# Optimization experiments

Measured on AMD Instinct MI355X. Metric: run time of the kernel, lower is better.

Reference implementation:

```python
import jax, jax.numpy as jnp
import numpy as np

B, IN_DIM, CTRL, N_LOC, LOC_SZ, OUT = 2048, 512, 512, 65536, 64, 1
EPS = 1e-8


def setup_inputs() -> dict:
    key = jax.random.key(0)
    ks = jax.random.split(key, 11)
    s = 0.02
    return {
        "x": jax.random.normal(ks[0], (B, IN_DIM), dtype=jnp.float32),
        # Controller: h = tanh(x W_h + b_h), gate = x W_g + b_g
        "W_h": jax.random.normal(ks[1], (IN_DIM, CTRL), dtype=jnp.float32) * s,
        "b_h": jnp.zeros((CTRL,), dtype=jnp.float32),
        "W_g": jax.random.normal(ks[2], (IN_DIM, 1), dtype=jnp.float32) * s,
        "b_g": jnp.zeros((1,), dtype=jnp.float32),
        # Head read-key net: key = tanh(h W_k + b_k)
        "W_k": jax.random.normal(ks[3], (CTRL, LOC_SZ), dtype=jnp.float32) * s,
        "b_k": jnp.zeros((LOC_SZ,), dtype=jnp.float32),
        # Memory matrix [locations, location_size]
        "M": jax.random.normal(ks[4], (N_LOC, LOC_SZ), dtype=jnp.float32),
        # Output linear: (ctrl_dim + location_size) -> output_dim
        "W_out": jax.random.normal(ks[5], (CTRL + LOC_SZ, OUT), dtype=jnp.float32) * s,
        "b_out": jnp.zeros((OUT,), dtype=jnp.float32),
    }


def reference(x, W_h, b_h, W_g, b_g, W_k, b_k, M, W_out, b_out):
    # Vectorized version of the original per-sample Python loop.
    h = jnp.tanh(x @ W_h + b_h)                # [B, ctrl_dim]
    gate = x @ W_g + b_g                       # [B, 1]
    read_key = jnp.tanh(h @ W_k + b_k)         # [B, loc_sz]
    # Cosine-similarity content addressing over memory rows.
    kn = read_key / (jnp.linalg.norm(read_key, axis=-1, keepdims=True) + EPS)
    Mn = M / (jnp.linalg.norm(M, axis=-1, keepdims=True) + EPS)
    sim = kn @ Mn.T                            # [B, locations]
    w_read = jax.nn.softmax(sim, axis=-1)      # [B, locations]
    r = w_read @ M                             # [B, loc_sz]
    feat = jnp.concatenate([h, r], axis=-1)    # [B, ctrl_dim + loc_sz]
    output = (feat @ W_out + b_out)[:, 0]      # [B]
    # Original returns last-iteration h, gate, w_read alongside output.
    return output, h[-1], gate[-1], w_read[-1]
```

## Files before the change

kernel.cpp:

```cpp
#include <hip/hip_runtime.h>

#define B_SZ 2048
#define IN_DIM 512
#define CTRL 512
#define N_LOC 65536
#define NSPLIT 128
#define EPSV 1e-8f
#define LOG2E 1.4426950408889634f

typedef __attribute__((ext_vector_type(8))) short bf16x8;
typedef __attribute__((ext_vector_type(4))) float f32x4;
typedef __attribute__((ext_vector_type(16))) float f32x16;
typedef __attribute__((ext_vector_type(4))) unsigned int u32x4;
typedef __attribute__((ext_vector_type(8))) unsigned short u16x8;

static __device__ __forceinline__ unsigned int cvtpk(float lo, float hi) {
  unsigned int r;
  asm("v_cvt_pk_bf16_f32 %0, %1, %2" : "=v"(r) : "v"(lo), "v"(hi));
  return r;
}
static __device__ __forceinline__ unsigned short f2bf_hw(float f) {
  return (unsigned short)(cvtpk(f, f) & 0xffffu);
}
static __device__ __forceinline__ float bf2f(unsigned short u) {
  return __builtin_bit_cast(float, ((unsigned int)u) << 16);
}
static __device__ __forceinline__ float exp2_fast(float x) {
  float r;
  asm("v_exp_f32 %0, %1" : "=v"(r) : "v"(x));
  return r;
}
static __device__ __forceinline__ void gld_lds16(const unsigned short* g, unsigned short* l) {
  __builtin_amdgcn_global_load_lds(
      (const __attribute__((address_space(1))) void*)g,
      (__attribute__((address_space(3))) void*)l, 16, 0, 0);
}

__global__ __launch_bounds__(256) void k_mega(const float* __restrict__ x,
                                              const float* __restrict__ Wh,
                                              const float* __restrict__ Wk,
                                              const float* __restrict__ M,
                                              const float* __restrict__ bh,
                                              unsigned short* __restrict__ Wkt,
                                              unsigned short* __restrict__ Mn_t,
                                              unsigned short* __restrict__ Mt_t,
                                              float* __restrict__ h) {
  const int bx = blockIdx.x, t = threadIdx.x;
  if (bx < 1024) {
    const int b = bx;
    const int c4 = t & 15, lg = t >> 4;
    float vv[4][4], ss[4];
#pragma unroll
    for (int r = 0; r < 4; r++) {
      const int loc = b * 64 + lg * 4 + r;
      const float4 f = *(const float4*)&M[(size_t)loc * 64 + c4 * 4];
      vv[r][0] = f.x; vv[r][1] = f.y; vv[r][2] = f.z; vv[r][3] = f.w;
      ss[r] = f.x * f.x + f.y * f.y + f.z * f.z + f.w * f.w;
    }
#pragma unroll
    for (int r = 0; r < 4; r++)
#pragma unroll
      for (int off = 1; off < 16; off <<= 1) ss[r] += __shfl_xor(ss[r], off);
#pragma unroll
    for (int r = 0; r < 4; r++) {
      const int rr = lg * 4 + r;
      const float s = (1.f / (sqrtf(ss[r]) + EPSV)) * LOG2E;
      uint2 u;
      u.x = cvtpk(vv[r][0] * s, vv[r][1] * s);
      u.y = cvtpk(vv[r][2] * s, vv[r][3] * s);
      const int pos = b * 4096 + rr * 64 + (((c4 >> 1) ^ (rr & 7)) * 8) + (c4 & 1) * 4;
      *(uint2*)&Mn_t[pos] = u;
    }
#pragma unroll
    for (int j = 0; j < 4; j++) {
      const int rr = c4 * 4 + j;
      uint2 u;
      u.x = cvtpk(vv[0][j], vv[1][j]);
      u.y = cvtpk(vv[2][j], vv[3][j]);
      const int pos = b * 4096 + rr * 64 + (((lg >> 1) ^ (rr & 7)) * 8) + (lg & 1) * 4;
      *(uint2*)&Mt_t[pos] = u;
    }
  } else if (bx < 1032) {
    __shared__ float ld[64][65];
    const int ti = bx - 1024;
#pragma unroll
    for (int i = 0; i < 4; i++) {
      const int c = t + i * 256;
      const int r = c >> 4, cc4 = (c & 15) * 4;
      const float4 v = *(const float4*)&Wk[(size_t)(ti * 64 + r) * 64 + cc4];
      ld[r][cc4] = v.x; ld[r][cc4 + 1] = v.y; ld[r][cc4 + 2] = v.z; ld[r][cc4 + 3] = v.w;
    }
    __syncthreads();
#pragma unroll
    for (int i = 0; i < 2; i++) {
      const int c = t + i * 256;
      const int col = c >> 3, k8 = (c & 7) * 8;
      u16x8 o;
#pragma unroll
      for (int j = 0; j < 4; j++) {
        unsigned int u = cvtpk(ld[k8 + 2 * j][col], ld[k8 + 2 * j + 1][col]);
        o[2 * j] = (unsigned short)u;
        o[2 * j + 1] = (unsigned short)(u >> 16);
      }
      *(u16x8*)&Wkt[(size_t)col * IN_DIM + ti * 64 + k8] = o;
    }
  } else {
    __shared__ __align__(16) unsigned short xs[64 * 40];
    __shared__ __align__(16) unsigned short whs[64 * 40];
    const int id2 = bx - 1032;
    const int bm = (id2 & 31) * 64, bn = (id2 >> 5) * 64;
    const int lane = t & 63, wv = t >> 6, lo = lane & 15, g = lane >> 4;
    f32x4 acc[4];
#pragma unroll
    for (int ct = 0; ct < 4; ct++) acc[ct] = (f32x4){0.f, 0.f, 0.f, 0.f};
    for (int k0 = 0; k0 < IN_DIM; k0 += 32) {
#pragma unroll
      for (int i = 0; i < 2; i++) {
        const int lin = t + i * 256;
        const int r = lin >> 3, q = lin & 7;
        const float4 v = *(const float4*)&x[(size_t)(bm + r) * IN_DIM + k0 + q * 4];
        uint2 u;
        u.x = cvtpk(v.x, v.y);
        u.y = cvtpk(v.z, v.w);
        *(uint2*)&xs[r * 40 + q * 4] = u;
      }
#pragma unroll
      for (int i = 0; i < 2; i++) {
        const int lin = t + i * 256;
        const int kk = lin >> 4, q = lin & 15;
        const float4 v = *(const float4*)&Wh[(size_t)(k0 + kk) * CTRL + bn + q * 4];
        const unsigned int a = cvtpk(v.x, v.y), b2 = cvtpk(v.z, v.w);
        whs[(q * 4 + 0) * 40 + kk] = (unsigned short)a;
        whs[(q * 4 + 1) * 40 + kk] = (unsigned short)(a >> 16);
        whs[(q * 4 + 2) * 40 + kk] = (unsigned short)b2;
        whs[(q * 4 + 3) * 40 + kk] = (unsigned short)(b2 >> 16);
      }
      __syncthreads();
      const bf16x8 afr = *(const bf16x8*)&xs[(16 * wv + lo) * 40 + 8 * g];
#pragma unroll
      for (int ct = 0; ct < 4; ct++) {
        const bf16x8 bfr = *(const bf16x8*)&whs[(16 * ct + lo) * 40 + 8 * g];
        acc[ct] = __builtin_amdgcn_mfma_f32_16x16x32_bf16(afr, bfr, acc[ct], 0, 0, 0);
      }
      __syncthreads();
    }
#pragma unroll
    for (int ct = 0; ct < 4; ct++)
#pragma unroll
      for (int q = 0; q < 4; q++) {
        const int row = bm + 16 * wv + 4 * g + q;
        const int col = bn + 16 * ct + lo;
        h[(size_t)row * CTRL + col] = tanhf(acc[ct][q] + bh[col]);
      }
  }
}

__global__ __launch_bounds__(256) void k_readkey(const float* __restrict__ h_,
                                                 const unsigned short* __restrict__ Wkt,
                                                 const float* __restrict__ bk,
                                                 const float* __restrict__ x,
                                                 const float* __restrict__ Wg,
                                                 const float* __restrict__ bg,
                                                 unsigned short* __restrict__ kn_bf,
                                                 float* __restrict__ out) {
  __shared__ float sAcc[4][32][65];
  __shared__ float red[4];
  const int t = threadIdx.x, lane = t & 63, w = t >> 6;
  const int l31 = lane & 31, hh = lane >> 5;
  if (blockIdx.x < 64) {
    const int row0 = blockIdx.x * 32;
    f32x16 acc[2];
    acc[0] = (f32x16)(0.f); acc[1] = (f32x16)(0.f);
#pragma unroll
    for (int kk = 0; kk < 8; kk++) {
      const int kb = 128 * w + 16 * kk + 8 * hh;
      const float4 a0 = *(const float4*)&h_[(size_t)(row0 + l31) * CTRL + kb];
      const float4 a1 = *(const float4*)&h_[(size_t)(row0 + l31) * CTRL + kb + 4];
      const u32x4 av = {cvtpk(a0.x, a0.y), cvtpk(a0.z, a0.w), cvtpk(a1.x, a1.y), cvtpk(a1.z, a1.w)};
      const bf16x8 afr = __builtin_bit_cast(bf16x8, av);
#pragma unroll
      for (int ct = 0; ct < 2; ct++) {
        const bf16x8 bfr = *(const bf16x8*)&Wkt[(size_t)(32 * ct + l31) * IN_DIM + kb];
        acc[ct] = __builtin_amdgcn_mfma_f32_32x32x16_bf16(afr, bfr, acc[ct], 0, 0, 0);
      }
    }
#pragma unroll
    for (int ct = 0; ct < 2; ct++)
#pragma unroll
      for (int r = 0; r < 16; r++)
        sAcc[w][(r & 3) + 8 * (r >> 2) + 4 * hh][32 * ct + l31] = acc[ct][r];
    __syncthreads();
    const int row = t >> 3, c8 = (t & 7) * 8;
    float v[8];
    float ss = 0.f;
#pragma unroll
    for (int j = 0; j < 8; j++) {
      const float s = sAcc[0][row][c8 + j] + sAcc[1][row][c8 + j] +
                      sAcc[2][row][c8 + j] + sAcc[3][row][c8 + j] + bk[c8 + j];
      v[j] = tanhf(s);
      ss += v[j] * v[j];
    }
    ss += __shfl_xor(ss, 1);
    ss += __shfl_xor(ss, 2);
    ss += __shfl_xor(ss, 4);
    const float inv = 1.f / (sqrtf(ss) + EPSV);
    u16x8 o;
#pragma unroll
    for (int j = 0; j < 4; j++) {
      const unsigned int u = cvtpk(v[2 * j] * inv, v[2 * j + 1] * inv);
      o[2 * j] = (unsigned short)u;
      o[2 * j + 1] = (unsigned short)(u >> 16);
    }
    *(u16x8*)&kn_bf[(size_t)(row0 + row) * 64 + c8] = o;
  } else {
    out[2048 + t] = h_[(size_t)(B_SZ - 1) * CTRL + t];
    out[2048 + 256 + t] = h_[(size_t)(B_SZ - 1) * CTRL + 256 + t];
    float p = x[(size_t)(B_SZ - 1) * IN_DIM + t] * Wg[t] +
              x[(size_t)(B_SZ - 1) * IN_DIM + 256 + t] * Wg[256 + t];
#pragma unroll
    for (int off = 32; off >= 1; off >>= 1) p += __shfl_xor(p, off);
    if ((t & 63) == 0) red[t >> 6] = p;
    __syncthreads();
    if (t == 0) out[2048 + 512] = red[0] + red[1] + red[2] + red[3] + bg[0];
  }
}

__global__ __launch_bounds__(256, 2) void k_attn(const unsigned short* __restrict__ kn_bf,
                                                 const unsigned short* __restrict__ Mn_t,
                                                 const unsigned short* __restrict__ Mt_t,
                                                 float* __restrict__ l_part,
                                                 unsigned short* __restrict__ r_bf,
                                                 float* __restrict__ wdump) {
  __shared__ __align__(16) unsigned short sMn[2][4096];
  __shared__ __align__(16) unsigned short sMt[2][4096];
  const int sp = blockIdx.x, rb = blockIdx.y;
  const int t = threadIdx.x, lane = t & 63, w = t >> 6;
  const int l31 = lane & 31, hh = lane >> 5, l7 = lane & 7;
  const int row0 = rb * 256 + 64 * w;

  bf16x8 bq[2][4];
#pragma unroll
  for (int rs = 0; rs < 2; rs++)
#pragma unroll
    for (int kk = 0; kk < 4; kk++)
      bq[rs][kk] =
          *(const bf16x8*)&kn_bf[(size_t)(row0 + 32 * rs + l31) * 64 + 16 * kk + 8 * hh];

  const int so = w * 1024 + lane * 8;
  const int lo0 = w * 1024;
  {
    const size_t gb = (size_t)(sp * 8) * 4096;
#pragma unroll
    for (int cc = 0; cc < 2; cc++) {
      gld_lds16(&Mn_t[gb + so + cc * 512], &sMn[0][lo0 + cc * 512]);
      gld_lds16(&Mt_t[gb + so + cc * 512], &sMt[0][lo0 + cc * 512]);
    }
  }
  asm volatile("s_waitcnt vmcnt(0)" ::: "memory");
  __syncthreads();

  f32x16 Racc[2][2];
#pragma unroll
  for (int rs = 0; rs < 2; rs++)
#pragma unroll
    for (int dt = 0; dt < 2; dt++) Racc[rs][dt] = (f32x16)(0.f);
  float lr0a = 0.f, lr0b = 0.f, lr1a = 0.f, lr1b = 0.f;

  for (int it = 0; it < 8; ++it) {
    const int cur = it & 1, nxt = cur ^ 1;
    if (it < 7) {
      const size_t gn = (size_t)(sp * 8 + it + 1) * 4096;
#pragma unroll
      for (int cc = 0; cc < 2; cc++) {
        gld_lds16(&Mn_t[gn + so + cc * 512], &sMn[nxt][lo0 + cc * 512]);
        gld_lds16(&Mt_t[gn + so + cc * 512], &sMt[nxt][lo0 + cc * 512]);
      }
    }

    f32x16 cst[2][2];
#pragma unroll
    for (int rs = 0; rs < 2; rs++)
#pragma unroll
      for (int lt = 0; lt < 2; lt++) cst[rs][lt] = (f32x16)(0.f);
    __builtin_amdgcn_s_setprio(1);
#pragma unroll
    for (int kk = 0; kk < 4; kk++) {
      const int koff = ((2 * kk + hh) ^ l7) * 8;
      const bf16x8 a0 = *(const bf16x8*)&sMn[cur][l31 * 64 + koff];
      const bf16x8 a1 = *(const bf16x8*)&sMn[cur][(32 + l31) * 64 + koff];
      cst[0][0] = __builtin_amdgcn_mfma_f32_32x32x16_bf16(a0, bq[0][kk], cst[0][0], 0, 0, 0);
      cst[0][1] = __builtin_amdgcn_mfma_f32_32x32x16_bf16(a1, bq[0][kk], cst[0][1], 0, 0, 0);
      cst[1][0] = __builtin_amdgcn_mfma_f32_32x32x16_bf16(a0, bq[1][kk], cst[1][0], 0, 0, 0);
      cst[1][1] = __builtin_amdgcn_mfma_f32_32x32x16_bf16(a1, bq[1][kk], cst[1][1], 0, 0, 0);
    }
    __builtin_amdgcn_s_setprio(0);

#pragma unroll
    for (int r = 0; r < 16; r++) {
      cst[0][0][r] = exp2_fast(cst[0][0][r]); lr0a += cst[0][0][r];
      cst[0][1][r] = exp2_fast(cst[0][1][r]); lr0b += cst[0][1][r];
      cst[1][0][r] = exp2_fast(cst[1][0][r]); lr1a += cst[1][0][r];
      cst[1][1][r] = exp2_fast(cst[1][1][r]); lr1b += cst[1][1][r];
    }

    if (rb == 7 && w == 3 && l31 == 31) {
#pragma unroll
      for (int lt = 0; lt < 2; lt++)
#pragma unroll
        for (int rr = 0; rr < 4; rr++)
          *(float4*)&wdump[sp * 512 + it * 64 + 32 * lt + 8 * rr + 4 * hh] =
              make_float4(cst[1][lt][4 * rr], cst[1][lt][4 * rr + 1], cst[1][lt][4 * rr + 2],
                          cst[1][lt][4 * rr + 3]);
    }

    __builtin_amdgcn_s_setprio(1);
#pragma unroll
    for (int kk = 0; kk < 4; kk++) {
      const int lt = kk >> 1, e8 = (kk & 1) * 8;
      const int koff = ((2 * kk + hh) ^ l7) * 8;
      const bf16x8 b0f = *(const bf16x8*)&sMt[cur][l31 * 64 + koff];
      const bf16x8 b1f = *(const bf16x8*)&sMt[cur][(32 + l31) * 64 + koff];
#pragma unroll
      for (int rs = 0; rs < 2; rs++) {
        const unsigned int p0 = cvtpk(cst[rs][lt][e8 + 0], cst[rs][lt][e8 + 1]);
        const unsigned int p1 = cvtpk(cst[rs][lt][e8 + 2], cst[rs][lt][e8 + 3]);
        const unsigned int p2 = cvtpk(cst[rs][lt][e8 + 4], cst[rs][lt][e8 + 5]);
        const unsigned int p3 = cvtpk(cst[rs][lt][e8 + 6], cst[rs][lt][e8 + 7]);
        auto s0 = __builtin_amdgcn_permlane32_swap(p2, p0, false, false);
        auto s1 = __builtin_amdgcn_permlane32_swap(p3, p1, false, false);
        const u32x4 aw = {(unsigned int)s0[1], (unsigned int)s1[1], (unsigned int)s0[0],
                          (unsigned int)s1[0]};
        const bf16x8 afr = __builtin_bit_cast(bf16x8, aw);
        Racc[rs][0] = __builtin_amdgcn_mfma_f32_32x32x16_bf16(afr, b0f, Racc[rs][0], 0, 0, 0);
        Racc[rs][1] = __builtin_amdgcn_mfma_f32_32x32x16_bf16(afr, b1f, Racc[rs][1], 0, 0, 0);
      }
    }
    __builtin_amdgcn_s_setprio(0);

    asm volatile("s_waitcnt vmcnt(0)" ::: "memory");
    __syncthreads();
  }

  float lr0 = lr0a + lr0b, lr1 = lr1a + lr1b;
  lr0 += __shfl_xor(lr0, 32);
  lr1 += __shfl_xor(lr1, 32);
  if (hh == 0) {
    l_part[(size_t)(row0 + l31) * NSPLIT + sp] = lr0;
    l_part[(size_t)(row0 + 32 + l31) * NSPLIT + sp] = lr1;
  }

#pragma unroll
  for (int rs = 0; rs < 2; rs++)
#pragma unroll
    for (int dt = 0; dt < 2; dt++)
#pragma unroll
      for (int r = 0; r < 16; r++) {
        const int brow = (r & 3) + 8 * (r >> 2) + 4 * hh;
        r_bf[((size_t)(row0 + 32 * rs + brow) * NSPLIT + sp) * 64 + 32 * dt + l31] =
            f2bf_hw(Racc[rs][dt][r]);
      }
}

__global__ __launch_bounds__(256) void k_post(const float* __restrict__ l_part,
                                              const unsigned short* __restrict__ r_bf,
                                              const float* __restrict__ h,
                                              const float* __restrict__ Wout,
                                              const float* __restrict__ bout,
                                              const float* __restrict__ wdump,
                                              float* __restrict__ out) {
  const int lane = threadIdx.x & 63, w = threadIdx.x >> 6;
  const int bx = blockIdx.x;
  if (bx < 512) {
    const int row = bx * 4 + w;
    float l = l_part[(size_t)row * NSPLIT + lane] + l_part[(size_t)row * NSPLIT + 64 + lane];
#pragma unroll
    for (int off = 32; off >= 1; off >>= 1) l += __shfl_xor(l, off);
    float rd = 0.f;
    for (int sp2 = 0; sp2 < NSPLIT; sp2++)
      rd += bf2f(r_bf[((size_t)row * NSPLIT + sp2) * 64 + lane]);
    rd /= l;
    float acc = Wout[CTRL + lane] * rd;
    for (int k = lane; k < CTRL; k += 64) acc += h[(size_t)row * CTRL + k] * Wout[k];
#pragma unroll
    for (int off = 32; off >= 1; off >>= 1) acc += __shfl_xor(acc, off);
    if (lane == 0) out[row] = acc + bout[0];
  } else {
    float l = l_part[(size_t)(B_SZ - 1) * NSPLIT + lane] +
              l_part[(size_t)(B_SZ - 1) * NSPLIT + 64 + lane];
#pragma unroll
    for (int off = 32; off >= 1; off >>= 1) l += __shfl_xor(l, off);
    const float rl = 1.f / l;
    const int i = ((bx - 512) * 256 + threadIdx.x) * 4;
    const float4 v = *(const float4*)&wdump[i];
    *(float4*)&out[2048 + 512 + 1 + i] = make_float4(v.x * rl, v.y * rl, v.z * rl, v.w * rl);
  }
}

extern "C" void kernel_launch(void* const* d_in, const int* in_sizes, int n_in,
                              void* d_out, int out_size, void* d_ws, size_t ws_size,
                              hipStream_t stream) {
  const float* x = (const float*)d_in[0];
  const float* Wh = (const float*)d_in[1];
  const float* bh = (const float*)d_in[2];
  const float* Wg = (const float*)d_in[3];
  const float* bg = (const float*)d_in[4];
  const float* Wk = (const float*)d_in[5];
  const float* bk = (const float*)d_in[6];
  const float* M = (const float*)d_in[7];
  const float* Wout = (const float*)d_in[8];
  const float* bout = (const float*)d_in[9];
  float* out = (float*)d_out;

  float* ws = (float*)d_ws;
  float* h = ws;
  float* l_part = h + 1048576;
  float* wdump = l_part + 262144;
  unsigned short* r_bf = (unsigned short*)(wdump + 65536);
  unsigned short* kn_bf = r_bf + 16777216;
  unsigned short* Mn_t = kn_bf + 131072;
  unsigned short* Mt_t = Mn_t + 4194304;
  unsigned short* Wkt = Mt_t + 4194304;

  hipLaunchKernelGGL(k_mega, dim3(1288), dim3(256), 0, stream,
                     x, Wh, Wk, M, bh, Wkt, Mn_t, Mt_t, h);
  hipLaunchKernelGGL(k_readkey, dim3(65), dim3(256), 0, stream,
                     h, Wkt, bk, x, Wg, bg, kn_bf, out);
  hipLaunchKernelGGL(k_attn, dim3(NSPLIT, 8), dim3(256), 0, stream,
                     kn_bf, Mn_t, Mt_t, l_part, r_bf, wdump);
  hipLaunchKernelGGL(k_post, dim3(512 + 64), dim3(256), 0, stream,
                     l_part, r_bf, h, Wout, bout, wdump, out);
}
```

Measured before the change: 85.32 us.

## Halve attention splits and prefetch memory tiles through registers instead of direct LDS loads

Cuts the number of location splits from 128 to 64, so each attention block processes 16 tiles instead of 8. This halves the partial-sum and partial-read buffers that the post kernel must reduce. The XOR swizzle moves from the preprocessing kernel into the attention kernel's LDS store, and the global_load_lds double buffering is replaced by register prefetch followed by an LDS write after compute. The bf16 packing of probabilities is hoisted before the PV MFMA loop, and setprio is narrowed to cover only the MFMA issue. The trade-off is fewer blocks (512) and higher register pressure in exchange for less reduction traffic.

```diff
diff --git a/kernel.cpp b/kernel.cpp
--- a/kernel.cpp
+++ b/kernel.cpp
@@ -4,7 +4,8 @@
 #define IN_DIM 512
 #define CTRL 512
 #define N_LOC 65536
-#define NSPLIT 128
+#define NSPLIT 64
+#define LPS (N_LOC / NSPLIT)
 #define EPSV 1e-8f
 #define LOG2E 1.4426950408889634f
 
@@ -29,11 +30,6 @@
   float r;
   asm("v_exp_f32 %0, %1" : "=v"(r) : "v"(x));
   return r;
-}
-static __device__ __forceinline__ void gld_lds16(const unsigned short* g, unsigned short* l) {
-  __builtin_amdgcn_global_load_lds(
-      (const __attribute__((address_space(1))) void*)g,
-      (__attribute__((address_space(3))) void*)l, 16, 0, 0);
 }
 
 __global__ __launch_bounds__(256) void k_mega(const float* __restrict__ x,
@@ -63,22 +59,18 @@
       for (int off = 1; off < 16; off <<= 1) ss[r] += __shfl_xor(ss[r], off);
 #pragma unroll
     for (int r = 0; r < 4; r++) {
-      const int rr = lg * 4 + r;
       const float s = (1.f / (sqrtf(ss[r]) + EPSV)) * LOG2E;
       uint2 u;
       u.x = cvtpk(vv[r][0] * s, vv[r][1] * s);
       u.y = cvtpk(vv[r][2] * s, vv[r][3] * s);
-      const int pos = b * 4096 + rr * 64 + (((c4 >> 1) ^ (rr & 7)) * 8) + (c4 & 1) * 4;
-      *(uint2*)&Mn_t[pos] = u;
+      *(uint2*)&Mn_t[(size_t)b * 4096 + (lg * 4 + r) * 64 + c4 * 4] = u;
     }
 #pragma unroll
     for (int j = 0; j < 4; j++) {
-      const int rr = c4 * 4 + j;
       uint2 u;
       u.x = cvtpk(vv[0][j], vv[1][j]);
       u.y = cvtpk(vv[2][j], vv[3][j]);
-      const int pos = b * 4096 + rr * 64 + (((lg >> 1) ^ (rr & 7)) * 8) + (lg & 1) * 4;
-      *(uint2*)&Mt_t[pos] = u;
+      *(uint2*)&Mt_t[(size_t)b * 4096 + (c4 * 4 + j) * 64 + lg * 4] = u;
     }
   } else if (bx < 1032) {
     __shared__ float ld[64][65];
@@ -246,17 +238,16 @@
       bq[rs][kk] =
           *(const bf16x8*)&kn_bf[(size_t)(row0 + 32 * rs + l31) * 64 + 16 * kk + 8 * hh];
 
-  const int so = w * 1024 + lane * 8;
-  const int lo0 = w * 1024;
+  const int c0 = t, c1 = t + 256;
+  const int r0 = c0 >> 3, d0 = r0 * 64 + (((c0 & 7) * 8) ^ ((r0 & 7) * 8));
+  const int r1 = c1 >> 3, d1 = r1 * 64 + (((c1 & 7) * 8) ^ ((r1 & 7) * 8));
   {
-    const size_t gb = (size_t)(sp * 8) * 4096;
-#pragma unroll
-    for (int cc = 0; cc < 2; cc++) {
-      gld_lds16(&Mn_t[gb + so + cc * 512], &sMn[0][lo0 + cc * 512]);
-      gld_lds16(&Mt_t[gb + so + cc * 512], &sMt[0][lo0 + cc * 512]);
-    }
-  }
-  asm volatile("s_waitcnt vmcnt(0)" ::: "memory");
+    const size_t gb = (size_t)(sp * 16) * 4096;
+    *(u16x8*)&sMn[0][d0] = *(const u16x8*)&Mn_t[gb + c0 * 8];
+    *(u16x8*)&sMn[0][d1] = *(const u16x8*)&Mn_t[gb + c1 * 8];
+    *(u16x8*)&sMt[0][d0] = *(const u16x8*)&Mt_t[gb + c0 * 8];
+    *(u16x8*)&sMt[0][d1] = *(const u16x8*)&Mt_t[gb + c1 * 8];
+  }
   __syncthreads();
 
   f32x16 Racc[2][2];
@@ -266,15 +257,15 @@
     for (int dt = 0; dt < 2; dt++) Racc[rs][dt] = (f32x16)(0.f);
   float lr0a = 0.f, lr0b = 0.f, lr1a = 0.f, lr1b = 0.f;
 
-  for (int it = 0; it < 8; ++it) {
-    const int cur = it & 1, nxt = cur ^ 1;
-    if (it < 7) {
-      const size_t gn = (size_t)(sp * 8 + it + 1) * 4096;
-#pragma unroll
-      for (int cc = 0; cc < 2; cc++) {
-        gld_lds16(&Mn_t[gn + so + cc * 512], &sMn[nxt][lo0 + cc * 512]);
-        gld_lds16(&Mt_t[gn + so + cc * 512], &sMt[nxt][lo0 + cc * 512]);
-      }
+  u16x8 rn0, rn1, rt0, rt1;
+  for (int it = 0; it < 16; ++it) {
+    const int cur = it & 1;
+    if (it < 15) {
+      const size_t gn = (size_t)(sp * 16 + it + 1) * 4096;
+      rn0 = *(const u16x8*)&Mn_t[gn + c0 * 8];
+      rn1 = *(const u16x8*)&Mn_t[gn + c1 * 8];
+      rt0 = *(const u16x8*)&Mt_t[gn + c0 * 8];
+      rt1 = *(const u16x8*)&Mt_t[gn + c1 * 8];
     }
 
     f32x16 cst[2][2];
@@ -308,36 +299,47 @@
       for (int lt = 0; lt < 2; lt++)
 #pragma unroll
         for (int rr = 0; rr < 4; rr++)
-          *(float4*)&wdump[sp * 512 + it * 64 + 32 * lt + 8 * rr + 4 * hh] =
+          *(float4*)&wdump[sp * 1024 + it * 64 + 32 * lt + 8 * rr + 4 * hh] =
               make_float4(cst[1][lt][4 * rr], cst[1][lt][4 * rr + 1], cst[1][lt][4 * rr + 2],
                           cst[1][lt][4 * rr + 3]);
     }
 
-    __builtin_amdgcn_s_setprio(1);
+    unsigned int pkq[2][2][8];
+#pragma unroll
+    for (int rs = 0; rs < 2; rs++)
+#pragma unroll
+      for (int lt = 0; lt < 2; lt++)
+#pragma unroll
+        for (int m = 0; m < 8; m++)
+          pkq[rs][lt][m] = cvtpk(cst[rs][lt][2 * m], cst[rs][lt][2 * m + 1]);
+
 #pragma unroll
     for (int kk = 0; kk < 4; kk++) {
-      const int lt = kk >> 1, e8 = (kk & 1) * 8;
+      const int lt = kk >> 1, e4 = (kk & 1) * 4;
       const int koff = ((2 * kk + hh) ^ l7) * 8;
       const bf16x8 b0f = *(const bf16x8*)&sMt[cur][l31 * 64 + koff];
       const bf16x8 b1f = *(const bf16x8*)&sMt[cur][(32 + l31) * 64 + koff];
+      __builtin_amdgcn_s_setprio(1);
 #pragma unroll
       for (int rs = 0; rs < 2; rs++) {
-        const unsigned int p0 = cvtpk(cst[rs][lt][e8 + 0], cst[rs][lt][e8 + 1]);
-        const unsigned int p1 = cvtpk(cst[rs][lt][e8 + 2], cst[rs][lt][e8 + 3]);
-        const unsigned int p2 = cvtpk(cst[rs][lt][e8 + 4], cst[rs][lt][e8 + 5]);
-        const unsigned int p3 = cvtpk(cst[rs][lt][e8 + 6], cst[rs][lt][e8 + 7]);
-        auto s0 = __builtin_amdgcn_permlane32_swap(p2, p0, false, false);
-        auto s1 = __builtin_amdgcn_permlane32_swap(p3, p1, false, false);
+        auto s0 = __builtin_amdgcn_permlane32_swap(pkq[rs][lt][e4 + 2], pkq[rs][lt][e4 + 0],
+                                                   false, false);
+        auto s1 = __builtin_amdgcn_permlane32_swap(pkq[rs][lt][e4 + 3], pkq[rs][lt][e4 + 1],
+                                                   false, false);
         const u32x4 aw = {(unsigned int)s0[1], (unsigned int)s1[1], (unsigned int)s0[0],
                           (unsigned int)s1[0]};
         const bf16x8 afr = __builtin_bit_cast(bf16x8, aw);
         Racc[rs][0] = __builtin_amdgcn_mfma_f32_32x32x16_bf16(afr, b0f, Racc[rs][0], 0, 0, 0);
         Racc[rs][1] = __builtin_amdgcn_mfma_f32_32x32x16_bf16(afr, b1f, Racc[rs][1], 0, 0, 0);
       }
-    }
-    __builtin_amdgcn_s_setprio(0);
-
-    asm volatile("s_waitcnt vmcnt(0)" ::: "memory");
+      __builtin_amdgcn_s_setprio(0);
+    }
+
+    if (it < 15) {
+      const int nxt = cur ^ 1;
+      *(u16x8*)&sMn[nxt][d0] = rn0; *(u16x8*)&sMn[nxt][d1] = rn1;
+      *(u16x8*)&sMt[nxt][d0] = rt0; *(u16x8*)&sMt[nxt][d1] = rt1;
+    }
     __syncthreads();
   }
 
@@ -372,7 +374,7 @@
   const int bx = blockIdx.x;
   if (bx < 512) {
     const int row = bx * 4 + w;
-    float l = l_part[(size_t)row * NSPLIT + lane] + l_part[(size_t)row * NSPLIT + 64 + lane];
+    float l = l_part[(size_t)row * NSPLIT + lane];
 #pragma unroll
     for (int off = 32; off >= 1; off >>= 1) l += __shfl_xor(l, off);
     float rd = 0.f;
@@ -385,8 +387,7 @@
     for (int off = 32; off >= 1; off >>= 1) acc += __shfl_xor(acc, off);
     if (lane == 0) out[row] = acc + bout[0];
   } else {
-    float l = l_part[(size_t)(B_SZ - 1) * NSPLIT + lane] +
-              l_part[(size_t)(B_SZ - 1) * NSPLIT + 64 + lane];
+    float l = l_part[(size_t)(B_SZ - 1) * NSPLIT + lane];
 #pragma unroll
     for (int off = 32; off >= 1; off >>= 1) l += __shfl_xor(l, off);
     const float rl = 1.f / l;
@@ -414,9 +415,9 @@
   float* ws = (float*)d_ws;
   float* h = ws;
   float* l_part = h + 1048576;
-  float* wdump = l_part + 262144;
+  float* wdump = l_part + 131072;
   unsigned short* r_bf = (unsigned short*)(wdump + 65536);
-  unsigned short* kn_bf = r_bf + 16777216;
+  unsigned short* kn_bf = r_bf + 8388608;
   unsigned short* Mn_t = kn_bf + 131072;
   unsigned short* Mt_t = Mn_t + 4194304;
   unsigned short* Wkt = Mt_t + 4194304;
```

Result: faster. 80.63 us (median of 2 runs) (-5.5%).
